# Kernel tuning notes

Hardware: AMD Instinct MI355X
Metric: run time of the kernel (lower is better)

## Reference

```python
import jax, jax.numpy as jnp
import numpy as np

INPUT_SIZE = 512


def setup_inputs() -> dict:
    key = jax.random.key(0)
    k1, k2, k3 = jax.random.split(key, 3)
    B, S, N = 2, 128, INPUT_SIZE
    x = jax.random.normal(k1, (B, S, N), dtype=jnp.float32)
    # Linear(input_size -> 2*input_size); xavier-ish scale, zero bias (per init_weights)
    W = jax.random.normal(k2, (2 * N, N), dtype=jnp.float32) * (1.0 / np.sqrt(N))
    b = jnp.zeros((2 * N,), dtype=jnp.float32)
    # standard-normal noise consumed by MVN.rsample (made explicit for determinism)
    eps = jax.random.normal(k3, (B, S, N), dtype=jnp.float32)
    return {"x": x, "W": W, "b": b, "eps": eps}


def reference(x, W, b, eps):
    n = INPUT_SIZE
    # gauss_parameter_generator: stats = x @ W^T + b  -> [B, S, 2n]
    stats = jnp.einsum("bsn,mn->bsm", x, W) + b
    # NOTE: per the source, the FIRST half is the (pre-softplus) std param and the
    # SECOND half is the mean (mu = stats[..., n:], std = softplus(stats[..., :n])).
    mu = stats[..., n:]
    var = jax.nn.softplus(stats[..., :n])  # used as the COVARIANCE diagonal by MVN
    # diag_embed(var) -> [B, S, n, n] dense covariance (faithful to original output)
    std_mat = var[..., :, None] * jnp.eye(n, dtype=var.dtype)
    # MVN(mu, cov=diag(var)).rsample() == mu + cholesky(diag(var)) @ eps
    # cholesky of a diagonal is elementwise sqrt -> fused O(n) form:
    sample = mu + jnp.sqrt(var) * eps
    return (sample, mu, std_mat)
```

## Files before the change

### kernel.cpp

```cpp
#include <hip/hip_runtime.h>
#include <math.h>

#define NDIM 512
#define NROWS 256
#define JBT 32
#define RBT 16
#define ROWB 1040
#define SMEM_W (80 * ROWB)
#define VT_OFF SMEM_W
#define MT_OFF (SMEM_W + 2176)

typedef __attribute__((ext_vector_type(8))) short short8;
typedef __attribute__((ext_vector_type(4))) float f32x4;

__device__ __forceinline__ unsigned short f2bf(float f) {
    unsigned u = __float_as_uint(f);
    return (unsigned short)((u + 0x7FFFu + ((u >> 16) & 1u)) >> 16);
}

__global__ __launch_bounds__(256) void gs_mfma(const float* __restrict__ x,
                                               const float* __restrict__ W,
                                               const float* __restrict__ b,
                                               const float* __restrict__ eps,
                                               float* __restrict__ out) {
    __shared__ __align__(16) char smem[SMEM_W + 2 * 2176];

    const int tid = threadIdx.x;
    const int jb  = blockIdx.x * JBT;
    const int rb  = blockIdx.y * RBT;

    #pragma unroll 4
    for (int it = 0; it < 40; ++it) {
        const int f   = it * 256 + tid;
        const int row = f >> 7;
        const int c4  = f & 127;
        const float* src;
        if (row < 64) {
            const int h  = row >> 5;
            const int jl = row & 31;
            src = W + (size_t)(h * NDIM + jb + jl) * NDIM;
        } else {
            src = x + (size_t)(rb + row - 64) * NDIM;
        }
        const float4 v = *(const float4*)(src + 4 * c4);
        const unsigned lo = (unsigned)f2bf(v.x) | ((unsigned)f2bf(v.y) << 16);
        const unsigned hi = (unsigned)f2bf(v.z) | ((unsigned)f2bf(v.w) << 16);
        *(uint2*)(smem + (size_t)row * ROWB + 8 * c4) = make_uint2(lo, hi);
    }
    __syncthreads();

    const int lane = tid & 63;
    const int wave = tid >> 6;
    const int h = wave >> 1;
    const int t = wave & 1;

    const char* Ab = smem + (size_t)(h * 32 + t * 16 + (lane & 15)) * ROWB
                          + ((lane >> 4) * 16);
    const char* Bb = smem + (size_t)(64 + (lane & 15)) * ROWB
                          + ((lane >> 4) * 16);

    f32x4 acc = {0.f, 0.f, 0.f, 0.f};
    #pragma unroll
    for (int ks = 0; ks < 16; ++ks) {
        const short8 av = *(const short8*)(Ab + ks * 64);
        const short8 bv = *(const short8*)(Bb + ks * 64);
        acc = __builtin_amdgcn_mfma_f32_16x16x32_bf16(av, bv, acc, 0, 0, 0);
    }

    float* vt = (float*)(smem + VT_OFF);
    float* mt = (float*)(smem + MT_OFF);
    {
        const int q  = lane >> 4;
        const int rl = lane & 15;
        float* dst = (h == 0) ? vt : mt;
        #pragma unroll
        for (int reg = 0; reg < 4; ++reg) {
            const int jl = t * 16 + q * 4 + reg;
            float s = acc[reg] + b[h * NDIM + jb + jl];
            if (h == 0) s = (s > 20.f) ? s : log1pf(expf(s));
            dst[jl * 17 + rl] = s;
        }
    }
    __syncthreads();

    float* out_sample = out;
    float* out_mu     = out + (size_t)NROWS * NDIM;
    float* out_std    = out + (size_t)2 * NROWS * NDIM;

    #pragma unroll
    for (int p = 0; p < 2; ++p) {
        const int jo = tid & 31;
        const int ro = (tid >> 5) + p * 8;
        const int j  = jb + jo;
        const int r  = rb + ro;
        const float var = vt[jo * 17 + ro];
        const float mu  = mt[jo * 17 + ro];
        const float smp = mu + sqrtf(var) * eps[(size_t)r * NDIM + j];
        out_sample[(size_t)r * NDIM + j] = smp;
        out_mu[(size_t)r * NDIM + j]     = mu;
        out_std[(size_t)r * NDIM * NDIM + (size_t)j * NDIM + j] = var;
    }
}

extern "C" void kernel_launch(void* const* d_in, const int* in_sizes, int n_in,
                              void* d_out, int out_size, void* d_ws, size_t ws_size,
                              hipStream_t stream) {
    const float* x   = (const float*)d_in[0];
    const float* W   = (const float*)d_in[1];
    const float* b   = (const float*)d_in[2];
    const float* eps = (const float*)d_in[3];
    float* out = (float*)d_out;

    dim3 grid(NDIM / JBT, NROWS / RBT);
    gs_mfma<<<grid, 256, 0, stream>>>(x, W, b, eps, out);
}
```

Measured before the change: 249.4 us.

## Halve output-column tile and split the K reduction across waves

The output-column tile shrinks from 32 to 16, which doubles the grid and cuts per-block shared memory. The four waves now split the 512-long K dimension in halves instead of each covering a separate column slice. Partial MFMA accumulators go to shared memory and are summed in a final pass that applies bias, softplus, sampling and the output writes. The aim is more blocks and better occupancy for this small GEMM. The cost is twice as much redundant x loading and bf16 conversion across blocks, plus an extra barrier and a reduction step.

```diff
diff --git a/kernel.cpp b/kernel.cpp
--- a/kernel.cpp
+++ b/kernel.cpp
@@ -3,12 +3,11 @@
 
 #define NDIM 512
 #define NROWS 256
-#define JBT 32
+#define JBT 16
 #define RBT 16
+#define TOTROWS 48
 #define ROWB 1040
-#define SMEM_W (80 * ROWB)
-#define VT_OFF SMEM_W
-#define MT_OFF (SMEM_W + 2176)
+#define SMEM_BYTES (TOTROWS * ROWB)
 
 typedef __attribute__((ext_vector_type(8))) short short8;
 typedef __attribute__((ext_vector_type(4))) float f32x4;
@@ -23,24 +22,23 @@
                                                const float* __restrict__ b,
                                                const float* __restrict__ eps,
                                                float* __restrict__ out) {
-    __shared__ __align__(16) char smem[SMEM_W + 2 * 2176];
+    __shared__ __align__(16) char smem[SMEM_BYTES];
 
     const int tid = threadIdx.x;
     const int jb  = blockIdx.x * JBT;
     const int rb  = blockIdx.y * RBT;
 
     #pragma unroll 4
-    for (int it = 0; it < 40; ++it) {
+    for (int it = 0; it < 24; ++it) {
         const int f   = it * 256 + tid;
         const int row = f >> 7;
         const int c4  = f & 127;
         const float* src;
-        if (row < 64) {
-            const int h  = row >> 5;
-            const int jl = row & 31;
-            src = W + (size_t)(h * NDIM + jb + jl) * NDIM;
+        if (row < 32) {
+            const int h = row >> 4;
+            src = W + (size_t)(h * NDIM + jb + (row & 15)) * NDIM;
         } else {
-            src = x + (size_t)(rb + row - 64) * NDIM;
+            src = x + (size_t)(rb + row - 32) * NDIM;
         }
         const float4 v = *(const float4*)(src + 4 * c4);
         const unsigned lo = (unsigned)f2bf(v.x) | ((unsigned)f2bf(v.y) << 16);
@@ -51,55 +49,52 @@
 
     const int lane = tid & 63;
     const int wave = tid >> 6;
-    const int h = wave >> 1;
-    const int t = wave & 1;
+    const int h  = wave >> 1;
+    const int ks = wave & 1;
 
-    const char* Ab = smem + (size_t)(h * 32 + t * 16 + (lane & 15)) * ROWB
-                          + ((lane >> 4) * 16);
-    const char* Bb = smem + (size_t)(64 + (lane & 15)) * ROWB
-                          + ((lane >> 4) * 16);
+    const char* Ab = smem + (size_t)(h * 16 + (lane & 15)) * ROWB
+                          + ks * 512 + ((lane >> 4) * 16);
+    const char* Bb = smem + (size_t)(32 + (lane & 15)) * ROWB
+                          + ks * 512 + ((lane >> 4) * 16);
 
     f32x4 acc = {0.f, 0.f, 0.f, 0.f};
     #pragma unroll
-    for (int ks = 0; ks < 16; ++ks) {
-        const short8 av = *(const short8*)(Ab + ks * 64);
-        const short8 bv = *(const short8*)(Bb + ks * 64);
+    for (int st = 0; st < 8; ++st) {
+        const short8 av = *(const short8*)(Ab + st * 64);
+        const short8 bv = *(const short8*)(Bb + st * 64);
         acc = __builtin_amdgcn_mfma_f32_16x16x32_bf16(av, bv, acc, 0, 0, 0);
     }
 
-    float* vt = (float*)(smem + VT_OFF);
-    float* mt = (float*)(smem + MT_OFF);
+    __syncthreads();
+
+    float* part = (float*)smem;
     {
-        const int q  = lane >> 4;
-        const int rl = lane & 15;
-        float* dst = (h == 0) ? vt : mt;
-        #pragma unroll
-        for (int reg = 0; reg < 4; ++reg) {
-            const int jl = t * 16 + q * 4 + reg;
-            float s = acc[reg] + b[h * NDIM + jb + jl];
-            if (h == 0) s = (s > 20.f) ? s : log1pf(expf(s));
-            dst[jl * 17 + rl] = s;
-        }
+        float* dst = part + (size_t)(h * 2 + ks) * 320 + lane * 5;
+        dst[0] = acc[0]; dst[1] = acc[1]; dst[2] = acc[2]; dst[3] = acc[3];
     }
     __syncthreads();
+
+    const int jo = tid & 15;
+    const int ro = tid >> 4;
+    const int ls = ((jo >> 2) * 16 + ro) * 5 + (jo & 3);
+
+    const float sv = part[0 * 320 + ls] + part[1 * 320 + ls] + b[jb + jo];
+    const float sm = part[2 * 320 + ls] + part[3 * 320 + ls] + b[NDIM + jb + jo];
+
+    const float var = (sv > 20.f) ? sv : log1pf(expf(sv));
+    const float mu  = sm;
+
+    const int j = jb + jo;
+    const int r = rb + ro;
 
     float* out_sample = out;
     float* out_mu     = out + (size_t)NROWS * NDIM;
     float* out_std    = out + (size_t)2 * NROWS * NDIM;
 
-    #pragma unroll
-    for (int p = 0; p < 2; ++p) {
-        const int jo = tid & 31;
-        const int ro = (tid >> 5) + p * 8;
-        const int j  = jb + jo;
-        const int r  = rb + ro;
-        const float var = vt[jo * 17 + ro];
-        const float mu  = mt[jo * 17 + ro];
-        const float smp = mu + sqrtf(var) * eps[(size_t)r * NDIM + j];
-        out_sample[(size_t)r * NDIM + j] = smp;
-        out_mu[(size_t)r * NDIM + j]     = mu;
-        out_std[(size_t)r * NDIM * NDIM + (size_t)j * NDIM + j] = var;
-    }
+    const float smp = mu + sqrtf(var) * eps[(size_t)r * NDIM + j];
+    out_sample[(size_t)r * NDIM + j] = smp;
+    out_mu[(size_t)r * NDIM + j]     = mu;
+    out_std[(size_t)r * NDIM * NDIM + (size_t)j * NDIM + j] = var;
 }
 
 extern "C" void kernel_launch(void* const* d_in, const int* in_sizes, int n_in,
```

New measurement: 247.2 us. No clear change (-0.9%).
